# Kernel tuning notes

Measured on AMD Instinct MI355X. Metric: run time of the kernel, lower is better.

Reference implementation:

```python
import jax, jax.numpy as jnp
import numpy as np

N = 100000  # nodes
E = 1600000  # edges
N_IN, N_H = 256, 128


def _norms(edge_src, edge_dst):
    ones = jnp.ones((E,), dtype=jnp.float32)
    out_deg = jax.ops.segment_sum(ones, edge_src, num_segments=N)
    in_deg = jax.ops.segment_sum(ones, edge_dst, num_segments=N)
    # DGL clamps degrees to >= 1 for norm='both'
    norm_src = jnp.clip(out_deg, 1.0, None) ** -0.5  # [N]
    norm_dst = jnp.clip(in_deg, 1.0, None) ** -0.5   # [N]
    return norm_src, norm_dst


def _graph_conv(h, W, b, edge_src, edge_dst, norm_src, norm_dst):
    # symmetric norm: D_out^{-1/2} A D_in^{-1/2}; W applied pre-aggregation
    h = h * norm_src[:, None]          # [N, d_in]
    h = h @ W                          # [N, d_out]
    msg = h[edge_src]                  # [E, d_out] gather
    agg = jax.ops.segment_sum(msg, edge_dst, num_segments=N)  # scatter-add
    agg = agg * norm_dst[:, None]
    return jax.nn.relu(agg + b)


def setup_inputs() -> dict:
    key = jax.random.key(0)
    ks = jax.random.split(key, 7)
    feat = jax.random.normal(ks[0], (1, N, N_IN), dtype=jnp.float32)
    edge_src = jax.random.randint(ks[1], (E,), 0, N, dtype=jnp.int32)
    edge_dst = jax.random.randint(ks[2], (E,), 0, N, dtype=jnp.int32)
    # Glorot-uniform weights as in DGL GraphConv reset_parameters
    lim1 = (6.0 / (N_IN + N_H)) ** 0.5
    lim2 = (6.0 / (N_H + N_H)) ** 0.5
    W1 = jax.random.uniform(ks[3], (N_IN, N_H), jnp.float32, -lim1, lim1)
    b1 = jnp.zeros((N_H,), dtype=jnp.float32)
    W2 = jax.random.uniform(ks[4], (N_H, N_H), jnp.float32, -lim2, lim2)
    b2 = jnp.zeros((N_H,), dtype=jnp.float32)
    return {"feat": feat, "W1": W1, "b1": b1, "W2": W2, "b2": b2,
            "edge_src": edge_src, "edge_dst": edge_dst}


def reference(feat, W1, b1, W2, b2, edge_src, edge_dst):
    h = feat.squeeze(0)  # [N, n_in]
    norm_src, norm_dst = _norms(edge_src, edge_dst)
    h = _graph_conv(h, W1, b1, edge_src, edge_dst, norm_src, norm_dst)
    h = _graph_conv(h, W2, b2, edge_src, edge_dst, norm_src, norm_dst)
    return h
```

## Files before the change

kernel.cpp:

```cpp
#include <hip/hip_runtime.h>
#include <hip/hip_bf16.h>

#define N_NODES 100000
#define N_EDGES 1600000
#define NBUCK 391
#define NBLK 256
#define CHUNK (N_EDGES / NBLK)
#define MATP (NBUCK * NBLK)

typedef float f32x4 __attribute__((ext_vector_type(4)));
typedef unsigned short u16x8 __attribute__((ext_vector_type(8)));
typedef _Float16 f16x8 __attribute__((ext_vector_type(8)));

__device__ __forceinline__ void wt_elem(const float* __restrict__ W,
                                        _Float16* __restrict__ WTf,
                                        int K, int i) {
    int col = i / K, k = i - col * K;
    WTf[i] = (_Float16)W[(size_t)k * 128 + col];
}

__global__ __launch_bounds__(256) void fused_setup(
    const int* __restrict__ esrc, const int* __restrict__ edst,
    int* __restrict__ cnt_mat,
    const float* __restrict__ W1, _Float16* __restrict__ WT1f,
    const float* __restrict__ W2, _Float16* __restrict__ WT2f)
{
    __shared__ int hd[NBUCK], hs[NBUCK];
    const int b = blockIdx.x, t = threadIdx.x;
    if (b < NBLK) {
        for (int i = t; i < NBUCK; i += 256) { hd[i] = 0; hs[i] = 0; }
        __syncthreads();
        const int e1 = (b + 1) * CHUNK;
        for (int e = b * CHUNK + t; e < e1; e += 256) {
            atomicAdd(&hd[edst[e] >> 8], 1);
            atomicAdd(&hs[esrc[e] >> 8], 1);
        }
        __syncthreads();
        for (int i = t; i < NBUCK; i += 256) {
            cnt_mat[i * NBLK + b] = hd[i];
            cnt_mat[MATP + i * NBLK + b] = hs[i];
        }
    } else {
        int i = (b - NBLK) * 256 + t;
        if (i < 128 * 256) {
            wt_elem(W1, WT1f, 256, i);
        } else {
            int j = i - 128 * 256;
            wt_elem(W2, WT2f, 128, j);
        }
    }
}

__global__ __launch_bounds__(1024) void scan_blocks(const int* __restrict__ counts,
                                                    int* __restrict__ out,
                                                    int* __restrict__ partials, int n) {
    __shared__ int tmp[1024];
    int i = blockIdx.x * 1024 + threadIdx.x;
    int v = (i < n) ? counts[i] : 0;
    tmp[threadIdx.x] = v;
    __syncthreads();
    for (int off = 1; off < 1024; off <<= 1) {
        int t = (threadIdx.x >= (unsigned)off) ? tmp[threadIdx.x - off] : 0;
        __syncthreads();
        tmp[threadIdx.x] += t;
        __syncthreads();
    }
    if (i < n) out[i] = tmp[threadIdx.x] - v;
    if (threadIdx.x == 1023) partials[blockIdx.x] = tmp[1023];
}

__global__ __launch_bounds__(256) void scan_partials(int* __restrict__ partials, int nb) {
    __shared__ int tmp[256];
    int t = threadIdx.x;
    int v = (t < nb) ? partials[t] : 0;
    tmp[t] = v;
    __syncthreads();
    for (int off = 1; off < 256; off <<= 1) {
        int u = (t >= off) ? tmp[t - off] : 0;
        __syncthreads();
        tmp[t] += u;
        __syncthreads();
    }
    if (t < nb) partials[t] = tmp[t] - v;
}

__device__ __forceinline__ int sm_at(const int* __restrict__ scan_mat,
                                     const int* __restrict__ partials, int i) {
    return scan_mat[i] + partials[i >> 10];
}

__global__ __launch_bounds__(256) void bucket_scatter(const int* __restrict__ esrc,
                                                      const int* __restrict__ edst,
                                                      const int* __restrict__ scan_mat,
                                                      const int* __restrict__ partials,
                                                      unsigned int* __restrict__ tmp) {
    __shared__ int cd[NBUCK], cs[NBUCK];
    const int b = blockIdx.x, t = threadIdx.x;
    for (int i = t; i < NBUCK; i += 256) {
        cd[i] = sm_at(scan_mat, partials, i * NBLK + b);
        cs[i] = sm_at(scan_mat, partials, MATP + i * NBLK + b);
    }
    __syncthreads();
    const int e1 = (b + 1) * CHUNK;
    for (int e = b * CHUNK + t; e < e1; e += 256) {
        int s = esrc[e], d = edst[e];
        int pd = atomicAdd(&cd[d >> 8], 1);
        tmp[pd] = ((unsigned int)(d & 255) << 17) | (unsigned int)s;
        int ps = atomicAdd(&cs[s >> 8], 1);
        tmp[ps] = (unsigned int)s;
    }
}

__global__ __launch_bounds__(256) void finalize_fused(
    const unsigned int* __restrict__ tmp,
    const int* __restrict__ scan_mat,
    const int* __restrict__ partials,
    int* __restrict__ rowptr,
    int* __restrict__ csr_src,
    float* __restrict__ ndst,
    float* __restrict__ nsrc)
{
    __shared__ int hist[256];
    __shared__ int scn[256];
    __shared__ int cur[256];
    const int bb = blockIdx.x, t = threadIdx.x;
    if (bb < NBUCK) {
        const int b = bb;
        const int beg = sm_at(scan_mat, partials, b * 256);
        const int end = sm_at(scan_mat, partials, (b + 1) * 256);
        hist[t] = 0;
        __syncthreads();
        for (int j = beg + t; j < end; j += 256)
            atomicAdd(&hist[tmp[j] >> 17], 1);
        __syncthreads();
        int v = hist[t];
        scn[t] = v;
        __syncthreads();
        for (int off = 1; off < 256; off <<= 1) {
            int u = (t >= off) ? scn[t - off] : 0;
            __syncthreads();
            scn[t] += u;
            __syncthreads();
        }
        int excl = scn[t] - v;
        int node = b * 256 + t;
        if (node <= N_NODES) rowptr[node] = beg + excl;
        if (node < N_NODES) ndst[node] = rsqrtf(fmaxf((float)v, 1.0f));
        cur[t] = beg + excl;
        __syncthreads();
        for (int j = beg + t; j < end; j += 256) {
            unsigned int x = tmp[j];
            int pos = atomicAdd(&cur[x >> 17], 1);
            csr_src[pos] = (int)(x & 0x1FFFFu);
        }
    } else {
        const int b = bb - NBUCK;
        const int beg = sm_at(scan_mat, partials, MATP + b * 256);
        const int end = (b < NBUCK - 1) ? sm_at(scan_mat, partials, MATP + (b + 1) * 256)
                                        : 2 * N_EDGES;
        hist[t] = 0;
        __syncthreads();
        for (int j = beg + t; j < end; j += 256)
            atomicAdd(&hist[tmp[j] & 255u], 1);
        __syncthreads();
        int node = b * 256 + t;
        if (node < N_NODES) nsrc[node] = rsqrtf(fmaxf((float)hist[t], 1.0f));
    }
}

template<int K, int ATERMS, typename AT>
__global__ __launch_bounds__(256) void gemm_mfma(
    const AT* __restrict__ A,
    const _Float16* __restrict__ WTf,
    const float* __restrict__ rowscale,
    _Float16* __restrict__ C16,
    int M)
{
    constexpr int ASTR = 520;
    constexpr int BSTR = 1032;
    __shared__ _Float16 Ah[4 * ASTR];
    __shared__ _Float16 Al[ATERMS == 2 ? 4 * ASTR : 8];
    __shared__ _Float16 Bf[4 * BSTR];

    const int tid = threadIdx.x;
    const int bm = blockIdx.x * 64;
    const int lane = tid & 63;
    const int wid = tid >> 6;
    const int wm = wid >> 1;
    const int wn = wid & 1;
    const int lr = lane & 15;
    const int lg = lane >> 4;

    const int st_ar = tid >> 2;
    const int st_s8 = tid & 3;
    const int a_row_g = bm + st_ar;

    f32x4 acc[2][4];
    #pragma unroll
    for (int i = 0; i < 2; ++i)
        #pragma unroll
        for (int j = 0; j < 4; ++j)
            acc[i][j] = (f32x4){0.f, 0.f, 0.f, 0.f};

    float avreg[8];
    f16x8 areg16;
    f16x8 bv[2];

    auto load_tile = [&](int k0) {
        if (a_row_g < M) {
            const AT* ap = &A[(size_t)a_row_g * K + k0 + st_s8 * 8];
            if constexpr (sizeof(AT) == 4) {
                float4 v0 = *reinterpret_cast<const float4*>(ap);
                float4 v1 = *reinterpret_cast<const float4*>(ap + 4);
                avreg[0] = v0.x; avreg[1] = v0.y; avreg[2] = v0.z; avreg[3] = v0.w;
                avreg[4] = v1.x; avreg[5] = v1.y; avreg[6] = v1.z; avreg[7] = v1.w;
            } else {
                areg16 = *reinterpret_cast<const f16x8*>(ap);
            }
        } else {
            if constexpr (sizeof(AT) == 4) {
                #pragma unroll
                for (int j = 0; j < 8; ++j) avreg[j] = 0.f;
            } else {
                #pragma unroll
                for (int j = 0; j < 8; ++j) areg16[j] = (_Float16)0.f;
            }
        }
        #pragma unroll
        for (int i = 0; i < 2; ++i) {
            int lin = tid + i * 256;
            int col = lin >> 2;
            int s8  = lin & 3;
            bv[i] = *reinterpret_cast<const f16x8*>(&WTf[(size_t)col * K + k0 + s8 * 8]);
        }
    };

    load_tile(0);

    for (int k0 = 0; k0 < K; k0 += 32) {
        {
            int off = st_s8 * ASTR + st_ar * 8;
            if constexpr (sizeof(AT) == 4) {
                f16x8 vh, vl;
                #pragma unroll
                for (int j = 0; j < 8; ++j) {
                    _Float16 h = (_Float16)avreg[j];
                    vh[j] = h;
                    vl[j] = (_Float16)(avreg[j] - (float)h);
                }
                *reinterpret_cast<f16x8*>(&Ah[off]) = vh;
                if constexpr (ATERMS == 2)
                    *reinterpret_cast<f16x8*>(&Al[off]) = vl;
            } else {
                *reinterpret_cast<f16x8*>(&Ah[off]) = areg16;
            }
            #pragma unroll
            for (int i = 0; i < 2; ++i) {
                int lin = tid + i * 256;
                int col = lin >> 2;
                int s8  = lin & 3;
                *reinterpret_cast<f16x8*>(&Bf[s8 * BSTR + col * 8]) = bv[i];
            }
        }
        __syncthreads();

        if (k0 + 32 < K) load_tile(k0 + 32);

        {
            f16x8 afh[2], afl[2], bf[4];
            #pragma unroll
            for (int mt = 0; mt < 2; ++mt) {
                int row = wm * 32 + mt * 16 + lr;
                int off = lg * ASTR + row * 8;
                afh[mt] = *reinterpret_cast<const f16x8*>(&Ah[off]);
                if constexpr (ATERMS == 2)
                    afl[mt] = *reinterpret_cast<const f16x8*>(&Al[off]);
            }
            #pragma unroll
            for (int nt = 0; nt < 4; ++nt) {
                int col = wn * 64 + nt * 16 + lr;
                bf[nt] = *reinterpret_cast<const f16x8*>(&Bf[lg * BSTR + col * 8]);
            }
            #pragma unroll
            for (int mt = 0; mt < 2; ++mt) {
                #pragma unroll
                for (int nt = 0; nt < 4; ++nt) {
                    acc[mt][nt] = __builtin_amdgcn_mfma_f32_16x16x32_f16(
                        afh[mt], bf[nt], acc[mt][nt], 0, 0, 0);
                    if constexpr (ATERMS == 2)
                        acc[mt][nt] = __builtin_amdgcn_mfma_f32_16x16x32_f16(
                            afl[mt], bf[nt], acc[mt][nt], 0, 0, 0);
                }
            }
        }
        __syncthreads();
    }

    #pragma unroll
    for (int mt = 0; mt < 2; ++mt) {
        #pragma unroll
        for (int r = 0; r < 4; ++r) {
            int row = bm + wm * 32 + mt * 16 + lg * 4 + r;
            if (row < M) {
                float s = rowscale[row];
                #pragma unroll
                for (int nt = 0; nt < 4; ++nt) {
                    int col = wn * 64 + nt * 16 + lr;
                    C16[(size_t)row * 128 + col] = (_Float16)(acc[mt][nt][r] * s);
                }
            }
        }
    }
}

template<typename OT>
__global__ __launch_bounds__(256) void aggregate_full(
    const _Float16* __restrict__ h16,
    const int* __restrict__ rowptr,
    const int* __restrict__ csr_src,
    const float* __restrict__ ndst,
    const float* __restrict__ bias,
    OT* __restrict__ out, int N, int half_blocks)
{
    int b = blockIdx.x;
    int c_base = 0;
    if (b >= half_blocks) { c_base = 64; b -= half_blocks; }
    int g = b * blockDim.x + threadIdx.x;
    int node = g >> 3;
    if (node >= N) return;
    int c8 = ((g & 7) * 8) + c_base;
    int beg = rowptr[node];
    int end = rowptr[node + 1];
    float acc[8] = {0.f, 0.f, 0.f, 0.f, 0.f, 0.f, 0.f, 0.f};
    int j = beg;
    for (; j + 3 < end; j += 4) {
        int s0 = csr_src[j];
        int s1 = csr_src[j + 1];
        int s2 = csr_src[j + 2];
        int s3 = csr_src[j + 3];
        f16x8 v0 = *reinterpret_cast<const f16x8*>(&h16[(size_t)s0 * 128 + c8]);
        f16x8 v1 = *reinterpret_cast<const f16x8*>(&h16[(size_t)s1 * 128 + c8]);
        f16x8 v2 = *reinterpret_cast<const f16x8*>(&h16[(size_t)s2 * 128 + c8]);
        f16x8 v3 = *reinterpret_cast<const f16x8*>(&h16[(size_t)s3 * 128 + c8]);
        #pragma unroll
        for (int k = 0; k < 8; ++k)
            acc[k] += ((float)v0[k] + (float)v1[k]) + ((float)v2[k] + (float)v3[k]);
    }
    for (; j < end; ++j) {
        int s0 = csr_src[j];
        f16x8 v0 = *reinterpret_cast<const f16x8*>(&h16[(size_t)s0 * 128 + c8]);
        #pragma unroll
        for (int k = 0; k < 8; ++k) acc[k] += (float)v0[k];
    }
    float sc = ndst[node];
    const float4 b0 = *reinterpret_cast<const float4*>(&bias[c8]);
    const float4 b1 = *reinterpret_cast<const float4*>(&bias[c8 + 4]);
    float r[8];
    r[0] = fmaxf(acc[0] * sc + b0.x, 0.f);
    r[1] = fmaxf(acc[1] * sc + b0.y, 0.f);
    r[2] = fmaxf(acc[2] * sc + b0.z, 0.f);
    r[3] = fmaxf(acc[3] * sc + b0.w, 0.f);
    r[4] = fmaxf(acc[4] * sc + b1.x, 0.f);
    r[5] = fmaxf(acc[5] * sc + b1.y, 0.f);
    r[6] = fmaxf(acc[6] * sc + b1.z, 0.f);
    r[7] = fmaxf(acc[7] * sc + b1.w, 0.f);
    OT* op = &out[(size_t)node * 128 + c8];
    if constexpr (sizeof(OT) == 4) {
        float4 r0 = {r[0], r[1], r[2], r[3]};
        float4 r1 = {r[4], r[5], r[6], r[7]};
        *reinterpret_cast<float4*>(op) = r0;
        *reinterpret_cast<float4*>(op + 4) = r1;
    } else {
        f16x8 rv;
        #pragma unroll
        for (int k = 0; k < 8; ++k) rv[k] = (_Float16)r[k];
        *reinterpret_cast<f16x8*>(op) = rv;
    }
}

extern "C" void kernel_launch(void* const* d_in, const int* in_sizes, int n_in,
                              void* d_out, int out_size, void* d_ws, size_t ws_size,
                              hipStream_t stream) {
    const float* feat = (const float*)d_in[0];
    const float* W1   = (const float*)d_in[1];
    const float* b1   = (const float*)d_in[2];
    const float* W2   = (const float*)d_in[3];
    const float* b2   = (const float*)d_in[4];
    const int* esrc   = (const int*)d_in[5];
    const int* edst   = (const int*)d_in[6];
    float* out = (float*)d_out;

    const int Nn = N_NODES, E = N_EDGES;
    const int SCAN_N = 2 * MATP;
    const int SCAN_NB = (SCAN_N + 1023) / 1024;

    float* hseg   = (float*)d_ws;
    _Float16* h16   = (_Float16*)hseg;
    _Float16* h1out = h16 + (size_t)Nn * 128;
    _Float16* WT1f = (_Float16*)(hseg + (size_t)Nn * 128);
    _Float16* WT2f = WT1f + 128 * 256;
    int* csr_src  = (int*)(WT2f + 128 * 128);
    int* rowptr   = csr_src + E;
    unsigned int* tmp = (unsigned int*)(rowptr + 100004);
    int* cnt_mat  = (int*)(tmp + 2 * (size_t)E);
    int* scan_mat = cnt_mat + SCAN_N;
    int* partials = scan_mat + SCAN_N;
    float* nsrc   = (float*)(partials + ((SCAN_NB + 3) & ~3));
    float* ndst   = nsrc + Nn;

    fused_setup<<<NBLK + 192, 256, 0, stream>>>(esrc, edst, cnt_mat, W1, WT1f, W2, WT2f);

    scan_blocks<<<SCAN_NB, 1024, 0, stream>>>(cnt_mat, scan_mat, partials, SCAN_N);
    scan_partials<<<1, 256, 0, stream>>>(partials, SCAN_NB);

    bucket_scatter<<<NBLK, 256, 0, stream>>>(esrc, edst, scan_mat, partials, tmp);
    finalize_fused<<<2 * NBUCK, 256, 0, stream>>>(tmp, scan_mat, partials,
                                                  rowptr, csr_src, ndst, nsrc);

    const int gemm_grid = (Nn + 63) / 64;
    const int aggh_grid = (Nn * 8 + 255) / 256;

    gemm_mfma<256, 2, float><<<gemm_grid, 256, 0, stream>>>(feat, WT1f, nsrc, h16, Nn);
    aggregate_full<_Float16><<<2 * aggh_grid, 256, 0, stream>>>(
        h16, rowptr, csr_src, ndst, b1, h1out, Nn, aggh_grid);

    gemm_mfma<128, 1, _Float16><<<gemm_grid, 256, 0, stream>>>(h1out, WT2f, nsrc, h16, Nn);
    aggregate_full<float><<<2 * aggh_grid, 256, 0, stream>>>(
        h16, rowptr, csr_src, ndst, b2, out, Nn, aggh_grid);
}
```

Baseline: 223.7 us.

## Fuse layer-1 aggregation with layer-2 GEMM in a single kernel

Replaces the separate first-layer aggregation kernel and second-layer GEMM with one kernel. Each block aggregates 64 nodes into shared memory, then multiplies them by W2 using MFMA. This removes the global round trip of the intermediate fp16 activations and one launch. In exchange, each thread gathers neighbors for four nodes in sequence and the kernel uses more shared memory, which may reduce the parallelism available to hide gather latency. The GEMM and aggregation templates are simplified to their single remaining instantiations.

```diff
diff --git a/kernel.cpp b/kernel.cpp
--- a/kernel.cpp
+++ b/kernel.cpp
@@ -168,9 +168,9 @@
     }
 }
 
-template<int K, int ATERMS, typename AT>
+template<int K>
 __global__ __launch_bounds__(256) void gemm_mfma(
-    const AT* __restrict__ A,
+    const float* __restrict__ A,
     const _Float16* __restrict__ WTf,
     const float* __restrict__ rowscale,
     _Float16* __restrict__ C16,
@@ -179,7 +179,7 @@
     constexpr int ASTR = 520;
     constexpr int BSTR = 1032;
     __shared__ _Float16 Ah[4 * ASTR];
-    __shared__ _Float16 Al[ATERMS == 2 ? 4 * ASTR : 8];
+    __shared__ _Float16 Al[4 * ASTR];
     __shared__ _Float16 Bf[4 * BSTR];
 
     const int tid = threadIdx.x;
@@ -203,28 +203,18 @@
             acc[i][j] = (f32x4){0.f, 0.f, 0.f, 0.f};
 
     float avreg[8];
-    f16x8 areg16;
     f16x8 bv[2];
 
     auto load_tile = [&](int k0) {
         if (a_row_g < M) {
-            const AT* ap = &A[(size_t)a_row_g * K + k0 + st_s8 * 8];
-            if constexpr (sizeof(AT) == 4) {
-                float4 v0 = *reinterpret_cast<const float4*>(ap);
-                float4 v1 = *reinterpret_cast<const float4*>(ap + 4);
-                avreg[0] = v0.x; avreg[1] = v0.y; avreg[2] = v0.z; avreg[3] = v0.w;
-                avreg[4] = v1.x; avreg[5] = v1.y; avreg[6] = v1.z; avreg[7] = v1.w;
-            } else {
-                areg16 = *reinterpret_cast<const f16x8*>(ap);
-            }
+            const float* ap = &A[(size_t)a_row_g * K + k0 + st_s8 * 8];
+            float4 v0 = *reinterpret_cast<const float4*>(ap);
+            float4 v1 = *reinterpret_cast<const float4*>(ap + 4);
+            avreg[0] = v0.x; avreg[1] = v0.y; avreg[2] = v0.z; avreg[3] = v0.w;
+            avreg[4] = v1.x; avreg[5] = v1.y; avreg[6] = v1.z; avreg[7] = v1.w;
         } else {
-            if constexpr (sizeof(AT) == 4) {
-                #pragma unroll
-                for (int j = 0; j < 8; ++j) avreg[j] = 0.f;
-            } else {
-                #pragma unroll
-                for (int j = 0; j < 8; ++j) areg16[j] = (_Float16)0.f;
-            }
+            #pragma unroll
+            for (int j = 0; j < 8; ++j) avreg[j] = 0.f;
         }
         #pragma unroll
         for (int i = 0; i < 2; ++i) {
@@ -240,20 +230,15 @@
     for (int k0 = 0; k0 < K; k0 += 32) {
         {
             int off = st_s8 * ASTR + st_ar * 8;
-            if constexpr (sizeof(AT) == 4) {
-                f16x8 vh, vl;
-                #pragma unroll
-                for (int j = 0; j < 8; ++j) {
-                    _Float16 h = (_Float16)avreg[j];
-                    vh[j] = h;
-                    vl[j] = (_Float16)(avreg[j] - (float)h);
-                }
-                *reinterpret_cast<f16x8*>(&Ah[off]) = vh;
-                if constexpr (ATERMS == 2)
-                    *reinterpret_cast<f16x8*>(&Al[off]) = vl;
-            } else {
-                *reinterpret_cast<f16x8*>(&Ah[off]) = areg16;
-            }
+            f16x8 vh, vl;
+            #pragma unroll
+            for (int j = 0; j < 8; ++j) {
+                _Float16 h = (_Float16)avreg[j];
+                vh[j] = h;
+                vl[j] = (_Float16)(avreg[j] - (float)h);
+            }
+            *reinterpret_cast<f16x8*>(&Ah[off]) = vh;
+            *reinterpret_cast<f16x8*>(&Al[off]) = vl;
             #pragma unroll
             for (int i = 0; i < 2; ++i) {
                 int lin = tid + i * 256;
@@ -273,8 +258,7 @@
                 int row = wm * 32 + mt * 16 + lr;
                 int off = lg * ASTR + row * 8;
                 afh[mt] = *reinterpret_cast<const f16x8*>(&Ah[off]);
-                if constexpr (ATERMS == 2)
-                    afl[mt] = *reinterpret_cast<const f16x8*>(&Al[off]);
+                afl[mt] = *reinterpret_cast<const f16x8*>(&Al[off]);
             }
             #pragma unroll
             for (int nt = 0; nt < 4; ++nt) {
@@ -287,9 +271,8 @@
                 for (int nt = 0; nt < 4; ++nt) {
                     acc[mt][nt] = __builtin_amdgcn_mfma_f32_16x16x32_f16(
                         afh[mt], bf[nt], acc[mt][nt], 0, 0, 0);
-                    if constexpr (ATERMS == 2)
-                        acc[mt][nt] = __builtin_amdgcn_mfma_f32_16x16x32_f16(
-                            afl[mt], bf[nt], acc[mt][nt], 0, 0, 0);
+                    acc[mt][nt] = __builtin_amdgcn_mfma_f32_16x16x32_f16(
+                        afl[mt], bf[nt], acc[mt][nt], 0, 0, 0);
                 }
             }
         }
@@ -313,14 +296,146 @@
     }
 }
 
-template<typename OT>
+__global__ __launch_bounds__(256) void fused_ag2(
+    const _Float16* __restrict__ h16,
+    const int* __restrict__ rowptr,
+    const int* __restrict__ csr_src,
+    const float* __restrict__ ndst,
+    const float* __restrict__ bias1,
+    const _Float16* __restrict__ WT2f,
+    const float* __restrict__ nsrc,
+    _Float16* __restrict__ h2,
+    int N)
+{
+    constexpr int ASTR = 520;
+    constexpr int BSTR = 1032;
+    __shared__ _Float16 Af[16 * ASTR];
+    __shared__ _Float16 Bf[16 * BSTR];
+
+    const int tid = threadIdx.x;
+    const int bm = blockIdx.x * 64;
+
+    #pragma unroll
+    for (int it = 0; it < 8; ++it) {
+        int e = it * 256 + tid;
+        int col = e >> 4;
+        int sk  = e & 15;
+        f16x8 v = *reinterpret_cast<const f16x8*>(&WT2f[(size_t)col * 128 + sk * 8]);
+        *reinterpret_cast<f16x8*>(&Bf[sk * BSTR + col * 8]) = v;
+    }
+
+    {
+        const int grp = tid >> 4;
+        const int l   = tid & 15;
+        const int c8  = l * 8;
+        const float4 bb0 = *reinterpret_cast<const float4*>(&bias1[c8]);
+        const float4 bb1 = *reinterpret_cast<const float4*>(&bias1[c8 + 4]);
+        #pragma unroll
+        for (int i = 0; i < 4; ++i) {
+            int rloc = grp * 4 + i;
+            int node = bm + rloc;
+            float acc[8] = {0.f, 0.f, 0.f, 0.f, 0.f, 0.f, 0.f, 0.f};
+            if (node < N) {
+                int beg = rowptr[node];
+                int end = rowptr[node + 1];
+                int j = beg;
+                for (; j + 3 < end; j += 4) {
+                    int s0 = csr_src[j];
+                    int s1 = csr_src[j + 1];
+                    int s2 = csr_src[j + 2];
+                    int s3 = csr_src[j + 3];
+                    f16x8 v0 = *reinterpret_cast<const f16x8*>(&h16[(size_t)s0 * 128 + c8]);
+                    f16x8 v1 = *reinterpret_cast<const f16x8*>(&h16[(size_t)s1 * 128 + c8]);
+                    f16x8 v2 = *reinterpret_cast<const f16x8*>(&h16[(size_t)s2 * 128 + c8]);
+                    f16x8 v3 = *reinterpret_cast<const f16x8*>(&h16[(size_t)s3 * 128 + c8]);
+                    #pragma unroll
+                    for (int k = 0; k < 8; ++k)
+                        acc[k] += ((float)v0[k] + (float)v1[k]) + ((float)v2[k] + (float)v3[k]);
+                }
+                for (; j < end; ++j) {
+                    int s0 = csr_src[j];
+                    f16x8 v0 = *reinterpret_cast<const f16x8*>(&h16[(size_t)s0 * 128 + c8]);
+                    #pragma unroll
+                    for (int k = 0; k < 8; ++k) acc[k] += (float)v0[k];
+                }
+                float sc = ndst[node];
+                acc[0] = fmaxf(acc[0] * sc + bb0.x, 0.f);
+                acc[1] = fmaxf(acc[1] * sc + bb0.y, 0.f);
+                acc[2] = fmaxf(acc[2] * sc + bb0.z, 0.f);
+                acc[3] = fmaxf(acc[3] * sc + bb0.w, 0.f);
+                acc[4] = fmaxf(acc[4] * sc + bb1.x, 0.f);
+                acc[5] = fmaxf(acc[5] * sc + bb1.y, 0.f);
+                acc[6] = fmaxf(acc[6] * sc + bb1.z, 0.f);
+                acc[7] = fmaxf(acc[7] * sc + bb1.w, 0.f);
+            }
+            f16x8 av;
+            #pragma unroll
+            for (int k = 0; k < 8; ++k) av[k] = (_Float16)acc[k];
+            *reinterpret_cast<f16x8*>(&Af[l * ASTR + rloc * 8]) = av;
+        }
+    }
+    __syncthreads();
+
+    const int lane = tid & 63;
+    const int wid = tid >> 6;
+    const int wm = wid >> 1;
+    const int wn = wid & 1;
+    const int lr = lane & 15;
+    const int lg = lane >> 4;
+
+    f32x4 acc[2][4];
+    #pragma unroll
+    for (int i = 0; i < 2; ++i)
+        #pragma unroll
+        for (int j = 0; j < 4; ++j)
+            acc[i][j] = (f32x4){0.f, 0.f, 0.f, 0.f};
+
+    #pragma unroll
+    for (int ks = 0; ks < 4; ++ks) {
+        const int slot = ks * 4 + lg;
+        f16x8 af[2], bf[4];
+        #pragma unroll
+        for (int mt = 0; mt < 2; ++mt) {
+            int row = wm * 32 + mt * 16 + lr;
+            af[mt] = *reinterpret_cast<const f16x8*>(&Af[slot * ASTR + row * 8]);
+        }
+        #pragma unroll
+        for (int nt = 0; nt < 4; ++nt) {
+            int col = wn * 64 + nt * 16 + lr;
+            bf[nt] = *reinterpret_cast<const f16x8*>(&Bf[slot * BSTR + col * 8]);
+        }
+        #pragma unroll
+        for (int mt = 0; mt < 2; ++mt)
+            #pragma unroll
+            for (int nt = 0; nt < 4; ++nt)
+                acc[mt][nt] = __builtin_amdgcn_mfma_f32_16x16x32_f16(
+                    af[mt], bf[nt], acc[mt][nt], 0, 0, 0);
+    }
+
+    #pragma unroll
+    for (int mt = 0; mt < 2; ++mt) {
+        #pragma unroll
+        for (int r = 0; r < 4; ++r) {
+            int row = bm + wm * 32 + mt * 16 + lg * 4 + r;
+            if (row < N) {
+                float s = nsrc[row];
+                #pragma unroll
+                for (int nt = 0; nt < 4; ++nt) {
+                    int col = wn * 64 + nt * 16 + lr;
+                    h2[(size_t)row * 128 + col] = (_Float16)(acc[mt][nt][r] * s);
+                }
+            }
+        }
+    }
+}
+
 __global__ __launch_bounds__(256) void aggregate_full(
     const _Float16* __restrict__ h16,
     const int* __restrict__ rowptr,
     const int* __restrict__ csr_src,
     const float* __restrict__ ndst,
     const float* __restrict__ bias,
-    OT* __restrict__ out, int N, int half_blocks)
+    float* __restrict__ out, int N, int half_blocks)
 {
     int b = blockIdx.x;
     int c_base = 0;
@@ -355,27 +470,18 @@
     float sc = ndst[node];
     const float4 b0 = *reinterpret_cast<const float4*>(&bias[c8]);
     const float4 b1 = *reinterpret_cast<const float4*>(&bias[c8 + 4]);
-    float r[8];
-    r[0] = fmaxf(acc[0] * sc + b0.x, 0.f);
-    r[1] = fmaxf(acc[1] * sc + b0.y, 0.f);
-    r[2] = fmaxf(acc[2] * sc + b0.z, 0.f);
-    r[3] = fmaxf(acc[3] * sc + b0.w, 0.f);
-    r[4] = fmaxf(acc[4] * sc + b1.x, 0.f);
-    r[5] = fmaxf(acc[5] * sc + b1.y, 0.f);
-    r[6] = fmaxf(acc[6] * sc + b1.z, 0.f);
-    r[7] = fmaxf(acc[7] * sc + b1.w, 0.f);
-    OT* op = &out[(size_t)node * 128 + c8];
-    if constexpr (sizeof(OT) == 4) {
-        float4 r0 = {r[0], r[1], r[2], r[3]};
-        float4 r1 = {r[4], r[5], r[6], r[7]};
-        *reinterpret_cast<float4*>(op) = r0;
-        *reinterpret_cast<float4*>(op + 4) = r1;
-    } else {
-        f16x8 rv;
-        #pragma unroll
-        for (int k = 0; k < 8; ++k) rv[k] = (_Float16)r[k];
-        *reinterpret_cast<f16x8*>(op) = rv;
-    }
+    float4 r0, r1;
+    r0.x = fmaxf(acc[0] * sc + b0.x, 0.f);
+    r0.y = fmaxf(acc[1] * sc + b0.y, 0.f);
+    r0.z = fmaxf(acc[2] * sc + b0.z, 0.f);
+    r0.w = fmaxf(acc[3] * sc + b0.w, 0.f);
+    r1.x = fmaxf(acc[4] * sc + b1.x, 0.f);
+    r1.y = fmaxf(acc[5] * sc + b1.y, 0.f);
+    r1.z = fmaxf(acc[6] * sc + b1.z, 0.f);
+    r1.w = fmaxf(acc[7] * sc + b1.w, 0.f);
+    float* op = &out[(size_t)node * 128 + c8];
+    *reinterpret_cast<float4*>(op) = r0;
+    *reinterpret_cast<float4*>(op + 4) = r1;
 }
 
 extern "C" void kernel_launch(void* const* d_in, const int* in_sizes, int n_in,
@@ -395,8 +501,8 @@
     const int SCAN_NB = (SCAN_N + 1023) / 1024;
 
     float* hseg   = (float*)d_ws;
-    _Float16* h16   = (_Float16*)hseg;
-    _Float16* h1out = h16 + (size_t)Nn * 128;
+    _Float16* h16 = (_Float16*)hseg;
+    _Float16* h2  = h16 + (size_t)Nn * 128;
     _Float16* WT1f = (_Float16*)(hseg + (size_t)Nn * 128);
     _Float16* WT2f = WT1f + 128 * 256;
     int* csr_src  = (int*)(WT2f + 128 * 128);
@@ -420,11 +526,11 @@
     const int gemm_grid = (Nn + 63) / 64;
     const int aggh_grid = (Nn * 8 + 255) / 256;
 
-    gemm_mfma<256, 2, float><<<gemm_grid, 256, 0, stream>>>(feat, WT1f, nsrc, h16, Nn);
-    aggregate_full<_Float16><<<2 * aggh_grid, 256, 0, stream>>>(
-        h16, rowptr, csr_src, ndst, b1, h1out, Nn, aggh_grid);
-
-    gemm_mfma<128, 1, _Float16><<<gemm_grid, 256, 0, stream>>>(h1out, WT2f, nsrc, h16, Nn);
-    aggregate_full<float><<<2 * aggh_grid, 256, 0, stream>>>(
-        h16, rowptr, csr_src, ndst, b2, out, Nn, aggh_grid);
-}
+    gemm_mfma<256><<<gemm_grid, 256, 0, stream>>>(feat, WT1f, nsrc, h16, Nn);
+
+    fused_ag2<<<gemm_grid, 256, 0, stream>>>(h16, rowptr, csr_src, ndst, b1,
+                                             WT2f, nsrc, h2, Nn);
+
+    aggregate_full<<<2 * aggh_grid, 256, 0, stream>>>(
+        h2, rowptr, csr_src, ndst, b2, out, Nn, aggh_grid);
+}
```

Result: slower. 244.1 us (+9.1%).
